# Kernel optimization log

Measured on AMD Instinct MI355X. Metric: run time of the kernel, lower is better.

Reference implementation:

```python
import jax, jax.numpy as jnp
import numpy as np

B, S, D, H = 32, 8192, 128, 256  # batch-of-MLPs, seq_len, emb_dim, hidden_dim
LN_EPS = 1e-5


def setup_inputs() -> dict:
    key = jax.random.key(0)
    k0, k1, k2, k3 = jax.random.split(key, 4)
    x = jax.random.normal(k0, (B, S, D), dtype=jnp.float32)
    # shared learned Q projection (torch Linear stores W as [out,in]; y = x @ W.T)
    Wq = jax.random.normal(k1, (D, D), dtype=jnp.float32) / np.float32(np.sqrt(D))
    # per-batch-index (non-shared) fast-weight MLP params
    W1 = jax.random.normal(k2, (B, D, H), dtype=jnp.float32) / np.float32(np.sqrt(D))
    b1 = jnp.zeros((B, H), dtype=jnp.float32)
    W2 = jax.random.normal(k3, (B, H, D), dtype=jnp.float32) / np.float32(np.sqrt(H))
    b2 = jnp.zeros((B, D), dtype=jnp.float32)
    gamma = jnp.ones((B, D), dtype=jnp.float32)
    beta = jnp.zeros((B, D), dtype=jnp.float32)
    return dict(x=x, Wq=Wq, W1=W1, b1=b1, W2=W2, b2=b2, gamma=gamma, beta=beta)


def reference(x, Wq, W1, b1, W2, b2, gamma, beta):
    # queries = silu(Q(x))
    q = jax.nn.silu(jnp.einsum('bsd,ed->bse', x, Wq))
    # torch F.normalize with default dim=1 -> L2-normalize over the sequence axis
    q = q / jnp.clip(jnp.linalg.norm(q, axis=1, keepdims=True), 1e-12)
    # ParallelMLPs: per-index MLP with distinct weights (grouped GEMM), + residual
    h = jax.nn.silu(jnp.einsum('bsd,bdh->bsh', q, W1) + b1[:, None, :])
    o = jnp.einsum('bsh,bhd->bsd', h, W2) + b2[:, None, :]
    mu = jnp.mean(o, axis=-1, keepdims=True)
    var = jnp.mean(jnp.square(o - mu), axis=-1, keepdims=True)
    ln = (o - mu) / jnp.sqrt(var + LN_EPS) * gamma[:, None, :] + beta[:, None, :]
    return ln + q
```

## Files before the change

### kernel.cpp

```cpp
#include <hip/hip_runtime.h>
#include <stdint.h>

#define B_ 32
#define S_ 8192
#define D_ 128
#define H_ 256

typedef __attribute__((ext_vector_type(4))) float f32x4;
typedef __attribute__((ext_vector_type(16))) float f32x16;
typedef __attribute__((ext_vector_type(8))) short bf16x8;
typedef __attribute__((ext_vector_type(4))) unsigned int u32x4;

__device__ __forceinline__ unsigned short f2bf(float f) {
    union { float f; unsigned int u; } v; v.f = f;
    unsigned int r = v.u + 0x7fffu + ((v.u >> 16) & 1u);
    return (unsigned short)(r >> 16);
}
__device__ __forceinline__ float bf2f(unsigned short u) {
    union { unsigned int u; float f; } v; v.u = ((unsigned int)u) << 16;
    return v.f;
}
__device__ __forceinline__ float silu_f(float v) {
    return v * __builtin_amdgcn_rcpf(1.0f + __expf(-v));
}
__device__ __forceinline__ unsigned int cvtpk(float lo, float hi) {
    unsigned int r;
    asm("v_cvt_pk_bf16_f32 %0, %1, %2" : "=v"(r) : "v"(lo), "v"(hi));
    return r;
}
__device__ __forceinline__ void plswap(unsigned int& a, unsigned int& b) {
    asm("v_permlane32_swap_b32 %0, %1" : "+v"(a), "+v"(b));
}
__device__ __forceinline__ void gl16(const void* g, void* l) {
    __builtin_amdgcn_global_load_lds(
        (const __attribute__((address_space(1))) unsigned int*)g,
        (__attribute__((address_space(3))) unsigned int*)l, 16, 0, 0);
}

__global__ void k_prep(const float* __restrict__ Wq, const float* __restrict__ W1,
                       const float* __restrict__ W2, const float* __restrict__ b1,
                       unsigned short* __restrict__ wq_bf,
                       unsigned short* __restrict__ wpkg,
                       float* __restrict__ b1r) {
    __shared__ __align__(16) unsigned short tile[8192];
    int t = threadIdx.x, blk = blockIdx.x;
    if (blk < 128) {
        int b = blk >> 2, hc = blk & 3;
#pragma unroll
        for (int i = 0; i < 8; i++) {
            int idx = t + i * 256;
            int d = idx >> 4, hj = idx & 15;
            f32x4 v = *(const f32x4*)(W1 + ((size_t)(b * D_ + d)) * H_ + hc * 64 + hj * 4);
#pragma unroll
            for (int u = 0; u < 4; u++) tile[(hj * 4 + u) * 128 + d] = f2bf(v[u]);
        }
        __syncthreads();
        char* img = (char*)wpkg + (size_t)b * 131072 + (size_t)hc * 32768;
#pragma unroll
        for (int i = 0; i < 4; i++) {
            int c = t + i * 256;
            int n = c >> 9, kk = (c >> 6) & 7, l = c & 63;
            u32x4 v = *(const u32x4*)(tile + (n * 32 + (l & 31)) * 128 + kk * 16 + (l >> 5) * 8);
            *(u32x4*)(img + n * 16384 + kk * 1024 + l * 16) = v;
        }
    } else if (blk < 256) {
        int a = blk - 128;
        int b = a >> 2, hc = a & 3;
#pragma unroll
        for (int i = 0; i < 8; i++) {
            int idx = t + i * 256;
            int h = idx >> 5, d4 = idx & 31;
            f32x4 v = *(const f32x4*)(W2 + ((size_t)(b * H_ + hc * 64 + h)) * D_ + d4 * 4);
#pragma unroll
            for (int u = 0; u < 4; u++) tile[(d4 * 4 + u) * 64 + h] = f2bf(v[u]);
        }
        __syncthreads();
        char* img = (char*)wpkg + (size_t)b * 131072 + (size_t)hc * 32768;
#pragma unroll
        for (int i = 0; i < 4; i++) {
            int c = t + i * 256;
            int dn = c >> 8, n = (c >> 7) & 1, kk2 = (c >> 6) & 1, l = c & 63;
            u32x4 v = *(const u32x4*)(tile + (dn * 32 + (l & 31)) * 64 + n * 32 + kk2 * 16 + (l >> 5) * 8);
            *(u32x4*)(img + n * 16384 + 8192 + dn * 2048 + kk2 * 1024 + l * 16) = v;
        }
    } else if (blk < 320) {
        int i = (blk - 256) * 256 + t;
        wq_bf[i] = f2bf(Wq[i]);
    } else {
        int idx = (blk - 320) * 256 + t;
        int b = idx >> 8, rem = idx & 255;
        int hc = rem >> 6, n = (rem >> 5) & 1, hi = (rem >> 4) & 1, r = rem & 15;
        int h = hc * 64 + n * 32 + (r & 3) + 8 * (r >> 2) + 4 * hi;
        b1r[idx] = b1[b * H_ + h];
    }
}

__global__ __launch_bounds__(256, 2) void k_qproj(
        const float* __restrict__ x, const unsigned short* __restrict__ wq_bf,
        unsigned short* __restrict__ q_img, float* __restrict__ part) {
    __shared__ __align__(16) unsigned short lds_a[128 * 128];
    __shared__ __align__(16) unsigned short lds_b[128 * 128];
    __shared__ float lds_ss[4][128];

    int tid = threadIdx.x;
    int lane = tid & 63, w = tid >> 6;
    int g = lane >> 4, c15 = lane & 15;
    int blk = blockIdx.x;
    int b = blk >> 6, st = blk & 63;
    size_t rowbase = (size_t)b * S_ + (size_t)st * 128;
    const float* xg = x + rowbase * D_;

    char* pA = (char*)lds_a;
    char* pB = (char*)lds_b;

#pragma unroll
    for (int i = 0; i < 8; i++) {
        int idx = tid + i * 256;
        int row = idx >> 4, cb = idx & 15;
        u32x4 v = *(const u32x4*)(wq_bf + row * 128 + cb * 8);
        *(u32x4*)(pB + row * 256 + (((unsigned)cb ^ (unsigned)(row & 7)) << 4)) = v;
    }
#pragma unroll
    for (int i = 0; i < 16; i++) {
        int idx = tid + i * 256;
        int row = idx >> 5, c4 = idx & 31;
        f32x4 v = *(const f32x4*)(xg + (size_t)row * 128 + c4 * 4);
        unsigned int lo = cvtpk(v[0], v[1]), hi2 = cvtpk(v[2], v[3]);
        *(unsigned long long*)(pA + row * 256 + ((c4 * 8) ^ ((row & 7) << 4))) =
            ((unsigned long long)hi2 << 32) | (unsigned long long)lo;
    }
    __syncthreads();

    f32x4 acc[2][8];
#pragma unroll
    for (int m = 0; m < 2; m++)
#pragma unroll
        for (int n = 0; n < 8; n++) acc[m][n] = (f32x4)0.0f;

#pragma unroll
    for (int kk = 0; kk < 4; kk++) {
        int kb = kk * 64 + (g << 4);
        bf16x8 a[2];
#pragma unroll
        for (int m = 0; m < 2; m++) {
            int row = (w << 5) + (m << 4) + c15;
            a[m] = *(const bf16x8*)(pA + row * 256 + (kb ^ ((row & 7) << 4)));
        }
#pragma unroll
        for (int n = 0; n < 8; n++) {
            int rowb = (n << 4) + c15;
            bf16x8 bb = *(const bf16x8*)(pB + rowb * 256 + (kb ^ ((rowb & 7) << 4)));
#pragma unroll
            for (int m = 0; m < 2; m++)
                acc[m][n] = __builtin_amdgcn_mfma_f32_16x16x32_bf16(a[m], bb, acc[m][n], 0, 0, 0);
        }
    }

    float ss[8];
#pragma unroll
    for (int n = 0; n < 8; n++) ss[n] = 0.0f;
#pragma unroll
    for (int m = 0; m < 2; m++)
#pragma unroll
        for (int n = 0; n < 8; n++)
#pragma unroll
            for (int r = 0; r < 4; r++) {
                float v = silu_f(acc[m][n][r]);
                acc[m][n][r] = v;
                ss[n] += v * v;
            }
#pragma unroll
    for (int n = 0; n < 8; n++) {
        float v = ss[n];
        v += __shfl_xor(v, 16, 64);
        v += __shfl_xor(v, 32, 64);
        if (lane < 16) lds_ss[w][(n << 4) + lane] = v;
    }
    __syncthreads();

#pragma unroll
    for (int m = 0; m < 2; m++)
#pragma unroll
        for (int n = 0; n < 8; n++)
#pragma unroll
            for (int r = 0; r < 4; r++) {
                int row = (w << 5) + (m << 4) + (g << 2) + r;
                int col = (n << 4) + c15;
                int byte = (row >> 5) * 8192 + (col >> 4) * 1024 +
                           ((row & 31) + ((col >> 3) & 1) * 32) * 16 + (col & 7) * 2;
                *(unsigned short*)(pA + byte) = f2bf(acc[m][n][r]);
            }
    __syncthreads();

    char* qo = (char*)q_img + ((size_t)(b * 256 + st * 4)) * 8192;
#pragma unroll
    for (int i = 0; i < 8; i++) {
        int off = tid * 16 + i * 4096;
        *(u32x4*)(qo + off) = *(const u32x4*)(pA + off);
    }
    if (tid < 128) {
        float s = lds_ss[0][tid] + lds_ss[1][tid] + lds_ss[2][tid] + lds_ss[3][tid];
        part[((size_t)b * 64 + st) * 128 + tid] = s;
    }
}

__global__ void k_scale(const float* __restrict__ part, float* __restrict__ scale) {
    int idx = blockIdx.x * 256 + threadIdx.x;
    int b = idx >> 7, e = idx & 127;
    const float* p = part + (size_t)b * 64 * 128 + e;
    float s = 0.0f;
    for (int t = 0; t < 64; t++) s += p[t * 128];
    scale[idx] = 1.0f / fmaxf(sqrtf(s), 1e-12f);
}

__global__ void k_wscale(unsigned short* __restrict__ wpkg, const float* __restrict__ scale) {
    int blk = blockIdx.x;
    int b = blk >> 2;
    char* region = (char*)wpkg + (size_t)b * 131072 + (size_t)(blk & 3) * 32768;
    int t = threadIdx.x;
#pragma unroll
    for (int i = 0; i < 4; i++) {
        int c = t + i * 256;
        int n = c >> 9, kk = (c >> 6) & 7, l = c & 63;
        char* addr = region + n * 16384 + kk * 1024 + l * 16;
        int d0 = kk * 16 + (l >> 5) * 8;
        u32x4 v = *(const u32x4*)addr;
        const unsigned short* pv = (const unsigned short*)&v;
        const float* sc = scale + b * D_ + d0;
        u32x4 o;
#pragma unroll
        for (int j = 0; j < 4; j++)
            o[j] = cvtpk(bf2f(pv[2 * j]) * sc[2 * j], bf2f(pv[2 * j + 1]) * sc[2 * j + 1]);
        *(u32x4*)addr = o;
    }
}

__global__ __launch_bounds__(256, 2) void k_mlp(
        const unsigned short* __restrict__ q_img, const float* __restrict__ scale,
        const unsigned short* __restrict__ wpkg, const float* __restrict__ b1r,
        const float* __restrict__ b2, const float* __restrict__ gamma,
        const float* __restrict__ beta, float* __restrict__ out) {
    __shared__ __align__(16) char lds[33792];
    int tid = threadIdx.x;
    int lane = tid & 63, w = tid >> 6;
    int c31 = lane & 31, hi = lane >> 5;
    int blk = blockIdx.x;
    int k = blk & 7, j = blk >> 3;
    int b = k * 4 + (j >> 6);
    int st = j & 63;

    const char* wb = (const char*)wpkg + (size_t)b * 131072;
    size_t grp = (size_t)b * 256 + st * 4 + w;
    const char* qg = (const char*)q_img + grp * 8192;

    bf16x8 qf[8];
#pragma unroll
    for (int kk = 0; kk < 8; kk++)
        qf[kk] = *(const bf16x8*)(qg + kk * 1024 + lane * 16);

    gl16((const char*)b1r + (size_t)b * 1024 + lane * 16, lds + 32768);

#define STAGEPKG(p, slot) do {                                          \
    _Pragma("unroll")                                                   \
    for (int i_ = 0; i_ < 4; i_++) {                                    \
        int off_ = tid * 16 + i_ * 4096;                                \
        gl16(wb + (p) * 16384 + off_, lds + (slot) * 16384 + off_);     \
    } } while (0)

    STAGEPKG(0, 0);
    STAGEPKG(1, 1);

    f32x16 acco[4];
#pragma unroll
    for (int dn = 0; dn < 4; dn++)
#pragma unroll
        for (int e = 0; e < 16; e++) acco[dn][e] = 0.0f;

    const float* b1l = (const float*)(lds + 32768);

#pragma unroll
    for (int p = 0; p < 8; p++) {
        const int hc = p >> 1, n = p & 1, slot = p & 1;
        if (p == 7) { asm volatile("s_waitcnt vmcnt(0)" ::: "memory"); }
        else        { asm volatile("s_waitcnt vmcnt(4)" ::: "memory"); }
        __builtin_amdgcn_s_barrier();
        __builtin_amdgcn_sched_barrier(0);

        f32x16 acch;
        {
            const float* bp = b1l + (hc * 2 + n) * 32 + hi * 16;
#pragma unroll
            for (int jq = 0; jq < 4; jq++) {
                f32x4 bq = *(const f32x4*)(bp + jq * 4);
#pragma unroll
                for (int e = 0; e < 4; e++) acch[jq * 4 + e] = bq[e];
            }
        }
        const char* s0 = lds + slot * 16384;
#pragma unroll
        for (int kk = 0; kk < 8; kk++) {
            bf16x8 wf = *(const bf16x8*)(s0 + kk * 1024 + lane * 16);
            acch = __builtin_amdgcn_mfma_f32_32x32x16_bf16(wf, qf[kk], acch, 0, 0, 0);
        }
        float sv[16];
#pragma unroll
        for (int r = 0; r < 16; r++) sv[r] = silu_f(acch[r]);
        unsigned int P[8];
#pragma unroll
        for (int pp = 0; pp < 8; pp++) P[pp] = cvtpk(sv[2 * pp], sv[2 * pp + 1]);
        plswap(P[0], P[2]); plswap(P[1], P[3]);
        plswap(P[4], P[6]); plswap(P[5], P[7]);
        union { unsigned int u[4]; bf16x8 v; } f0, f1;
        f0.u[0] = P[0]; f0.u[1] = P[1]; f0.u[2] = P[2]; f0.u[3] = P[3];
        f1.u[0] = P[4]; f1.u[1] = P[5]; f1.u[2] = P[6]; f1.u[3] = P[7];
        bf16x8 pa0 = f0.v, pa1 = f1.v;
#pragma unroll
        for (int kk2 = 0; kk2 < 2; kk2++)
#pragma unroll
            for (int dn = 0; dn < 4; dn++) {
                bf16x8 wf2 = *(const bf16x8*)(s0 + 8192 + dn * 2048 + kk2 * 1024 + lane * 16);
                acco[dn] = __builtin_amdgcn_mfma_f32_32x32x16_bf16(kk2 ? pa1 : pa0, wf2,
                                                                   acco[dn], 0, 0, 0);
            }

        asm volatile("s_waitcnt lgkmcnt(0)" ::: "memory");
        __builtin_amdgcn_sched_barrier(0);
        __builtin_amdgcn_s_barrier();
        if (p < 6) STAGEPKG(p + 2, slot);
    }
#undef STAGEPKG

    __syncthreads();
    char* myq = (char*)lds + w * 8192;
#pragma unroll
    for (int kk = 0; kk < 8; kk++)
        *(bf16x8*)(myq + c31 * 256 + ((kk * 32 + hi * 16) ^ ((c31 & 7) << 4))) = qf[kk];

    float scv[4], gv[4], bev[4], b2v[4];
#pragma unroll
    for (int dn = 0; dn < 4; dn++) {
        int d = dn * 32 + c31;
        scv[dn] = scale[b * 128 + d];
        gv[dn]  = gamma[b * 128 + d];
        bev[dn] = beta[b * 128 + d];
        b2v[dn] = b2[b * 128 + d];
    }

    float* og = out + grp * 32 * 128;
#pragma unroll
    for (int r = 0; r < 16; r++) {
        float v0 = acco[0][r] + b2v[0], v1 = acco[1][r] + b2v[1];
        float v2 = acco[2][r] + b2v[2], v3 = acco[3][r] + b2v[3];
        float s1 = (v0 + v1) + (v2 + v3);
        float s2 = (v0 * v0 + v1 * v1) + (v2 * v2 + v3 * v3);
        s1 += __shfl_xor(s1, 1, 64);   s2 += __shfl_xor(s2, 1, 64);
        s1 += __shfl_xor(s1, 2, 64);   s2 += __shfl_xor(s2, 2, 64);
        s1 += __shfl_xor(s1, 4, 64);   s2 += __shfl_xor(s2, 4, 64);
        s1 += __shfl_xor(s1, 8, 64);   s2 += __shfl_xor(s2, 8, 64);
        s1 += __shfl_xor(s1, 16, 64);  s2 += __shfl_xor(s2, 16, 64);
        float mu = s1 * (1.0f / 128.0f);
        float var = s2 * (1.0f / 128.0f) - mu * mu;
        float rstd = rsqrtf(var + 1e-5f);
        int srow0 = (r & 3) + 8 * (r >> 2);
        int row = srow0 + 4 * hi;
        float vv[4] = {v0, v1, v2, v3};
#pragma unroll
        for (int dn = 0; dn < 4; dn++) {
            float qv = bf2f(*(const unsigned short*)(myq + row * 256 +
                        ((dn * 64 + c31 * 2) ^ ((row & 7) << 4)))) * scv[dn];
            float o = (vv[dn] - mu) * rstd * gv[dn] + bev[dn] + qv;
            og[(size_t)row * 128 + dn * 32 + c31] = o;
        }
    }
}

extern "C" void kernel_launch(void* const* d_in, const int* in_sizes, int n_in,
                              void* d_out, int out_size, void* d_ws, size_t ws_size,
                              hipStream_t stream) {
    (void)in_sizes; (void)n_in; (void)out_size; (void)ws_size;
    const float* x     = (const float*)d_in[0];
    const float* Wq    = (const float*)d_in[1];
    const float* W1    = (const float*)d_in[2];
    const float* b1    = (const float*)d_in[3];
    const float* W2    = (const float*)d_in[4];
    const float* b2    = (const float*)d_in[5];
    const float* gamma = (const float*)d_in[6];
    const float* beta  = (const float*)d_in[7];
    float* out = (float*)d_out;

    char* ws = (char*)d_ws;
    unsigned short* wq_bf = (unsigned short*)(ws);
    unsigned short* wpkg  = (unsigned short*)(ws + 32768);
    float* part           = (float*)(ws + 4227072);
    float* scale          = (float*)(ws + 5275648);
    float* b1r            = (float*)(ws + 5292032);
    unsigned short* q_img = (unsigned short*)(ws + 5324800);

    hipLaunchKernelGGL(k_prep, dim3(352), dim3(256), 0, stream, Wq, W1, W2, b1, wq_bf, wpkg, b1r);
    hipLaunchKernelGGL(k_qproj, dim3(2048), dim3(256), 0, stream, x, wq_bf, q_img, part);
    hipLaunchKernelGGL(k_scale, dim3(16), dim3(256), 0, stream, part, scale);
    hipLaunchKernelGGL(k_wscale, dim3(128), dim3(256), 0, stream, wpkg, scale);
    hipLaunchKernelGGL(k_mlp, dim3(2048), dim3(256), 0, stream,
                       q_img, scale, wpkg, b1r, b2, gamma, beta, out);
}
```

Before: 132.7 us.

## Restructure Q-projection to 32x32 MFMA with pre-packed Wq fragments and fused scale kernel

Wq is now packed in k_prep straight into the 32x32x16 MFMA fragment layout. k_qproj computes the transposed product with Wq as the A operand, streamed from global/L2, and x held in registers. It writes the q image directly from registers using permlane32 swaps, so the LDS staging of Wq and the LDS-based output transpose are gone. The scale reduction and weight-scaling kernels are merged into one launch that recomputes the per-batch column norms in each block. The trade-offs are many cross-lane shuffles for the sum of squares, Wq fetched from global memory per wave, a launch bound of 1 instead of 2, and redundant norm reductions across the four blocks per batch.

```diff
diff --git a/kernel.cpp b/kernel.cpp
--- a/kernel.cpp
+++ b/kernel.cpp
@@ -39,7 +39,7 @@
 
 __global__ void k_prep(const float* __restrict__ Wq, const float* __restrict__ W1,
                        const float* __restrict__ W2, const float* __restrict__ b1,
-                       unsigned short* __restrict__ wq_bf,
+                       unsigned short* __restrict__ wq_img,
                        unsigned short* __restrict__ wpkg,
                        float* __restrict__ b1r) {
     __shared__ __align__(16) unsigned short tile[8192];
@@ -83,11 +83,22 @@
             u32x4 v = *(const u32x4*)(tile + (dn * 32 + (l & 31)) * 64 + n * 32 + kk2 * 16 + (l >> 5) * 8);
             *(u32x4*)(img + n * 16384 + 8192 + dn * 2048 + kk2 * 1024 + l * 16) = v;
         }
-    } else if (blk < 320) {
-        int i = (blk - 256) * 256 + t;
-        wq_bf[i] = f2bf(Wq[i]);
+    } else if (blk < 260) {
+        int base = (blk - 256) * 512;
+#pragma unroll
+        for (int i = 0; i < 2; i++) {
+            int c = base + i * 256 + t;
+            int n = c >> 9, kk = (c >> 6) & 7, l = c & 63;
+            int e = n * 32 + (l & 31), d = kk * 16 + (l >> 5) * 8;
+            f32x4 v0 = *(const f32x4*)(Wq + e * 128 + d);
+            f32x4 v1 = *(const f32x4*)(Wq + e * 128 + d + 4);
+            u32x4 o;
+            o[0] = cvtpk(v0[0], v0[1]); o[1] = cvtpk(v0[2], v0[3]);
+            o[2] = cvtpk(v1[0], v1[1]); o[3] = cvtpk(v1[2], v1[3]);
+            *(u32x4*)((char*)wq_img + (size_t)c * 16) = o;
+        }
     } else {
-        int idx = (blk - 320) * 256 + t;
+        int idx = (blk - 260) * 256 + t;
         int b = idx >> 8, rem = idx & 255;
         int hc = rem >> 6, n = (rem >> 5) & 1, hi = (rem >> 4) & 1, r = rem & 15;
         int h = hc * 64 + n * 32 + (r & 3) + 8 * (r >> 2) + 4 * hi;
@@ -95,129 +106,106 @@
     }
 }
 
-__global__ __launch_bounds__(256, 2) void k_qproj(
-        const float* __restrict__ x, const unsigned short* __restrict__ wq_bf,
+__global__ __launch_bounds__(256, 1) void k_qproj(
+        const float* __restrict__ x, const unsigned short* __restrict__ wq_img,
         unsigned short* __restrict__ q_img, float* __restrict__ part) {
-    __shared__ __align__(16) unsigned short lds_a[128 * 128];
-    __shared__ __align__(16) unsigned short lds_b[128 * 128];
-    __shared__ float lds_ss[4][128];
-
+    __shared__ __align__(16) char lds[32768];
     int tid = threadIdx.x;
     int lane = tid & 63, w = tid >> 6;
-    int g = lane >> 4, c15 = lane & 15;
+    int c31 = lane & 31, hi = lane >> 5;
     int blk = blockIdx.x;
     int b = blk >> 6, st = blk & 63;
     size_t rowbase = (size_t)b * S_ + (size_t)st * 128;
     const float* xg = x + rowbase * D_;
 
-    char* pA = (char*)lds_a;
-    char* pB = (char*)lds_b;
-
-#pragma unroll
-    for (int i = 0; i < 8; i++) {
-        int idx = tid + i * 256;
-        int row = idx >> 4, cb = idx & 15;
-        u32x4 v = *(const u32x4*)(wq_bf + row * 128 + cb * 8);
-        *(u32x4*)(pB + row * 256 + (((unsigned)cb ^ (unsigned)(row & 7)) << 4)) = v;
-    }
 #pragma unroll
     for (int i = 0; i < 16; i++) {
         int idx = tid + i * 256;
         int row = idx >> 5, c4 = idx & 31;
         f32x4 v = *(const f32x4*)(xg + (size_t)row * 128 + c4 * 4);
         unsigned int lo = cvtpk(v[0], v[1]), hi2 = cvtpk(v[2], v[3]);
-        *(unsigned long long*)(pA + row * 256 + ((c4 * 8) ^ ((row & 7) << 4))) =
+        *(unsigned long long*)(lds + row * 256 + ((c4 * 8) ^ ((row & 7) << 4))) =
             ((unsigned long long)hi2 << 32) | (unsigned long long)lo;
     }
     __syncthreads();
 
-    f32x4 acc[2][8];
-#pragma unroll
-    for (int m = 0; m < 2; m++)
-#pragma unroll
-        for (int n = 0; n < 8; n++) acc[m][n] = (f32x4)0.0f;
-
-#pragma unroll
-    for (int kk = 0; kk < 4; kk++) {
-        int kb = kk * 64 + (g << 4);
-        bf16x8 a[2];
-#pragma unroll
-        for (int m = 0; m < 2; m++) {
-            int row = (w << 5) + (m << 4) + c15;
-            a[m] = *(const bf16x8*)(pA + row * 256 + (kb ^ ((row & 7) << 4)));
-        }
-#pragma unroll
-        for (int n = 0; n < 8; n++) {
-            int rowb = (n << 4) + c15;
-            bf16x8 bb = *(const bf16x8*)(pB + rowb * 256 + (kb ^ ((rowb & 7) << 4)));
-#pragma unroll
-            for (int m = 0; m < 2; m++)
-                acc[m][n] = __builtin_amdgcn_mfma_f32_16x16x32_bf16(a[m], bb, acc[m][n], 0, 0, 0);
-        }
-    }
-
-    float ss[8];
-#pragma unroll
-    for (int n = 0; n < 8; n++) ss[n] = 0.0f;
-#pragma unroll
-    for (int m = 0; m < 2; m++)
-#pragma unroll
-        for (int n = 0; n < 8; n++)
-#pragma unroll
-            for (int r = 0; r < 4; r++) {
-                float v = silu_f(acc[m][n][r]);
-                acc[m][n][r] = v;
-                ss[n] += v * v;
-            }
-#pragma unroll
-    for (int n = 0; n < 8; n++) {
-        float v = ss[n];
-        v += __shfl_xor(v, 16, 64);
-        v += __shfl_xor(v, 32, 64);
-        if (lane < 16) lds_ss[w][(n << 4) + lane] = v;
+    bf16x8 xf[8];
+#pragma unroll
+    for (int kk = 0; kk < 8; kk++)
+        xf[kk] = *(const bf16x8*)(lds + (w * 32 + c31) * 256 +
+                                  ((kk * 32 + hi * 16) ^ ((lane & 7) << 4)));
+
+    size_t grp = (size_t)b * 256 + st * 4 + w;
+    char* qo = (char*)q_img + grp * 8192;
+    float* ssl = (float*)(lds + w * 8192);
+
+#pragma unroll
+    for (int n = 0; n < 4; n++) {
+        f32x16 acch;
+#pragma unroll
+        for (int e = 0; e < 16; e++) acch[e] = 0.0f;
+#pragma unroll
+        for (int kk = 0; kk < 8; kk++) {
+            bf16x8 wqf = *(const bf16x8*)((const char*)wq_img + n * 8192 + kk * 1024 + lane * 16);
+            acch = __builtin_amdgcn_mfma_f32_32x32x16_bf16(wqf, xf[kk], acch, 0, 0, 0);
+        }
+        float sv[16];
+#pragma unroll
+        for (int r = 0; r < 16; r++) sv[r] = silu_f(acch[r]);
+        unsigned int P[8];
+#pragma unroll
+        for (int pp = 0; pp < 8; pp++) P[pp] = cvtpk(sv[2 * pp], sv[2 * pp + 1]);
+        plswap(P[0], P[2]); plswap(P[1], P[3]);
+        plswap(P[4], P[6]); plswap(P[5], P[7]);
+        union { unsigned int u[4]; bf16x8 v; } f0, f1;
+        f0.u[0] = P[0]; f0.u[1] = P[1]; f0.u[2] = P[2]; f0.u[3] = P[3];
+        f1.u[0] = P[4]; f1.u[1] = P[5]; f1.u[2] = P[6]; f1.u[3] = P[7];
+        *(bf16x8*)(qo + (2 * n) * 1024 + lane * 16) = f0.v;
+        *(bf16x8*)(qo + (2 * n + 1) * 1024 + lane * 16) = f1.v;
+        float ssq[16];
+#pragma unroll
+        for (int r = 0; r < 16; r++) ssq[r] = sv[r] * sv[r];
+#pragma unroll
+        for (int r = 0; r < 16; r++) {
+            ssq[r] += __shfl_xor(ssq[r], 1, 64);
+            ssq[r] += __shfl_xor(ssq[r], 2, 64);
+            ssq[r] += __shfl_xor(ssq[r], 4, 64);
+            ssq[r] += __shfl_xor(ssq[r], 8, 64);
+            ssq[r] += __shfl_xor(ssq[r], 16, 64);
+        }
+#pragma unroll
+        for (int r = 0; r < 16; r++) {
+            int dloc = (r & 3) + 8 * (r >> 2) + 4 * hi;
+            if ((lane & 31) == r) ssl[n * 32 + dloc] = ssq[r];
+        }
     }
     __syncthreads();
-
-#pragma unroll
-    for (int m = 0; m < 2; m++)
-#pragma unroll
-        for (int n = 0; n < 8; n++)
-#pragma unroll
-            for (int r = 0; r < 4; r++) {
-                int row = (w << 5) + (m << 4) + (g << 2) + r;
-                int col = (n << 4) + c15;
-                int byte = (row >> 5) * 8192 + (col >> 4) * 1024 +
-                           ((row & 31) + ((col >> 3) & 1) * 32) * 16 + (col & 7) * 2;
-                *(unsigned short*)(pA + byte) = f2bf(acc[m][n][r]);
-            }
-    __syncthreads();
-
-    char* qo = (char*)q_img + ((size_t)(b * 256 + st * 4)) * 8192;
-#pragma unroll
-    for (int i = 0; i < 8; i++) {
-        int off = tid * 16 + i * 4096;
-        *(u32x4*)(qo + off) = *(const u32x4*)(pA + off);
-    }
     if (tid < 128) {
-        float s = lds_ss[0][tid] + lds_ss[1][tid] + lds_ss[2][tid] + lds_ss[3][tid];
+        float s = *(const float*)(lds + 0 * 8192 + tid * 4) +
+                  *(const float*)(lds + 1 * 8192 + tid * 4) +
+                  *(const float*)(lds + 2 * 8192 + tid * 4) +
+                  *(const float*)(lds + 3 * 8192 + tid * 4);
         part[((size_t)b * 64 + st) * 128 + tid] = s;
     }
 }
 
-__global__ void k_scale(const float* __restrict__ part, float* __restrict__ scale) {
-    int idx = blockIdx.x * 256 + threadIdx.x;
-    int b = idx >> 7, e = idx & 127;
-    const float* p = part + (size_t)b * 64 * 128 + e;
-    float s = 0.0f;
-    for (int t = 0; t < 64; t++) s += p[t * 128];
-    scale[idx] = 1.0f / fmaxf(sqrtf(s), 1e-12f);
-}
-
-__global__ void k_wscale(unsigned short* __restrict__ wpkg, const float* __restrict__ scale) {
+__global__ void k_scalew(const float* __restrict__ part, unsigned short* __restrict__ wpkg,
+                         float* __restrict__ scale) {
+    __shared__ float sc_l[128];
     int blk = blockIdx.x;
     int b = blk >> 2;
+    int t = threadIdx.x;
+    if (t < 128) {
+        const float* p = part + (size_t)b * 8192 + t;
+        float s = 0.0f;
+#pragma unroll 8
+        for (int i = 0; i < 64; i++) s += p[i * 128];
+        float sc = 1.0f / fmaxf(sqrtf(s), 1e-12f);
+        sc_l[t] = sc;
+        if ((blk & 3) == 0) scale[b * 128 + t] = sc;
+    }
+    __syncthreads();
     char* region = (char*)wpkg + (size_t)b * 131072 + (size_t)(blk & 3) * 32768;
-    int t = threadIdx.x;
 #pragma unroll
     for (int i = 0; i < 4; i++) {
         int c = t + i * 256;
@@ -226,11 +214,11 @@
         int d0 = kk * 16 + (l >> 5) * 8;
         u32x4 v = *(const u32x4*)addr;
         const unsigned short* pv = (const unsigned short*)&v;
-        const float* sc = scale + b * D_ + d0;
         u32x4 o;
 #pragma unroll
         for (int j = 0; j < 4; j++)
-            o[j] = cvtpk(bf2f(pv[2 * j]) * sc[2 * j], bf2f(pv[2 * j + 1]) * sc[2 * j + 1]);
+            o[j] = cvtpk(bf2f(pv[2 * j]) * sc_l[d0 + 2 * j],
+                         bf2f(pv[2 * j + 1]) * sc_l[d0 + 2 * j + 1]);
         *(u32x4*)addr = o;
     }
 }
@@ -389,17 +377,16 @@
     float* out = (float*)d_out;
 
     char* ws = (char*)d_ws;
-    unsigned short* wq_bf = (unsigned short*)(ws);
-    unsigned short* wpkg  = (unsigned short*)(ws + 32768);
-    float* part           = (float*)(ws + 4227072);
-    float* scale          = (float*)(ws + 5275648);
-    float* b1r            = (float*)(ws + 5292032);
-    unsigned short* q_img = (unsigned short*)(ws + 5324800);
-
-    hipLaunchKernelGGL(k_prep, dim3(352), dim3(256), 0, stream, Wq, W1, W2, b1, wq_bf, wpkg, b1r);
-    hipLaunchKernelGGL(k_qproj, dim3(2048), dim3(256), 0, stream, x, wq_bf, q_img, part);
-    hipLaunchKernelGGL(k_scale, dim3(16), dim3(256), 0, stream, part, scale);
-    hipLaunchKernelGGL(k_wscale, dim3(128), dim3(256), 0, stream, wpkg, scale);
+    unsigned short* wq_img = (unsigned short*)(ws);
+    unsigned short* wpkg   = (unsigned short*)(ws + 32768);
+    float* part            = (float*)(ws + 4227072);
+    float* scale           = (float*)(ws + 5275648);
+    float* b1r             = (float*)(ws + 5292032);
+    unsigned short* q_img  = (unsigned short*)(ws + 5324800);
+
+    hipLaunchKernelGGL(k_prep, dim3(292), dim3(256), 0, stream, Wq, W1, W2, b1, wq_img, wpkg, b1r);
+    hipLaunchKernelGGL(k_qproj, dim3(2048), dim3(256), 0, stream, x, wq_img, q_img, part);
+    hipLaunchKernelGGL(k_scalew, dim3(128), dim3(256), 0, stream, part, wpkg, scale);
     hipLaunchKernelGGL(k_mlp, dim3(2048), dim3(256), 0, stream,
                        q_img, scale, wpkg, b1r, b2, gamma, beta, out);
 }
```

Measured after the change: 144.9 us. +9.2%, slower.
